# Kernel tuning notes

Hardware: AMD Instinct MI355X
Metric: run time of the kernel (lower is better)

The kernel has to match this reference:

```python
import jax, jax.numpy as jnp
import numpy as np

COMMITMENT_COST = 0.25
N_EMBED = 1024
EMB_DIM = 256

def setup_inputs() -> dict:
    key = jax.random.key(0)
    k1, k2 = jax.random.split(key)
    z = jax.random.normal(k1, (32, EMB_DIM, 32, 32), dtype=jnp.float32)
    # embedding.weight.data.uniform_(-1/n_embed, 1/n_embed)
    embedding = jax.random.uniform(k2, (N_EMBED, EMB_DIM), dtype=jnp.float32,
                                   minval=-1.0 / N_EMBED, maxval=1.0 / N_EMBED)
    return {"z": z, "embedding": embedding}

def reference(z, embedding):
    # NCHW -> NHWC
    zp = jnp.transpose(z, (0, 2, 3, 1))            # [B,H,W,D]
    in_shape = zp.shape
    flat = zp.reshape(-1, in_shape[-1])            # [N,D]
    # squared L2 distances (argmin equivalent to p=2 cdist argmin)
    d2 = (jnp.sum(flat * flat, axis=1, keepdims=True)
          - 2.0 * (flat @ embedding.T)
          + jnp.sum(embedding * embedding, axis=1))  # [N,K]
    idx = jnp.argmin(d2, axis=1)                   # [N]
    # one-hot @ codebook == direct gather
    z_quant = embedding[idx].reshape(in_shape)     # [B,H,W,D]
    codebook_loss = jnp.mean((z_quant - jax.lax.stop_gradient(zp)) ** 2)
    commitment_loss = jnp.mean((zp - jax.lax.stop_gradient(z_quant)) ** 2)
    loss = codebook_loss + COMMITMENT_COST * commitment_loss
    # straight-through estimator
    z_st = zp + jax.lax.stop_gradient(z_quant - zp)
    z_st = jnp.transpose(z_st, (0, 3, 1, 2))       # NHWC -> NCHW
    return (z_st, loss, codebook_loss, commitment_loss)
```

## Files before the change

### kernel.cpp

```cpp
#include <hip/hip_runtime.h>
#include <hip/hip_bf16.h>
#include <stdint.h>


typedef short v8s __attribute__((ext_vector_type(8)));
typedef float v4f __attribute__((ext_vector_type(4)));

__device__ inline unsigned short f2bf(float f) {
    uint32_t u = __float_as_uint(f);
    return (unsigned short)((u + 0x7fffu + ((u >> 16) & 1u)) >> 16);
}

__global__ __launch_bounds__(256) void k_prep_e(const float* __restrict__ E,
                                                v8s* __restrict__ Esw,
                                                float* __restrict__ nE,
                                                float* __restrict__ accum,
                                                unsigned* __restrict__ done) {
    __shared__ float Ef[16][264];
    int q = blockIdx.x, tid = threadIdx.x;
    const float4* Ein = (const float4*)(E + ((size_t)q << 12));
#pragma unroll
    for (int i = 0; i < 4; i++) {
        int f4 = i * 256 + tid;
        int row = f4 >> 6, c4 = (f4 & 63) << 2;
        *(float4*)&Ef[row][c4] = Ein[f4];
    }
    __syncthreads();
    {
        int c = tid >> 4, l = tid & 15;
        float s = 0.f;
#pragma unroll
        for (int j = 0; j < 16; j++) { float v = Ef[c][l + 16 * j]; s += v * v; }
#pragma unroll
        for (int off = 1; off < 16; off <<= 1) s += __shfl_xor(s, off);
        if (l == 0) nE[q * 16 + c] = 0.5f * s;
    }
#pragma unroll
    for (int i = 0; i < 2; i++) {
        int u = tid + i * 256;
        int um = u & 15, ug = (u >> 4) & 3, udc = (u >> 6) & 7;
        int d0 = udc * 32 + ug * 8;
        union { v8s v; unsigned short s[8]; } pk;
#pragma unroll
        for (int e = 0; e < 8; e++) pk.s[e] = f2bf(Ef[um][d0 + e]);
        Esw[((size_t)q << 9) + u] = pk.v;
    }
    if (q == 0 && tid == 0) { accum[0] = 0.f; done[0] = 0u; }
}

__global__ __launch_bounds__(512) void k_main(
        const v8s* __restrict__ Esw,
        const float* __restrict__ nE,
        const float* __restrict__ z,
        const float* __restrict__ E,
        float* __restrict__ out,
        float* __restrict__ accum,
        unsigned* __restrict__ done) {
    __shared__ union {
        v8s    B[2][4096];
        float4 Eg4[2048];
    } S;
    __shared__ float nEl[1024];
    __shared__ float nrmLds[128];
    __shared__ int   idxLds[128];
    __shared__ float w8[8];

    int tid = threadIdx.x;
    int lane = tid & 63, w = tid >> 6;
    int g = lane >> 4, m = lane & 15;
    int R0 = blockIdx.x << 7;
    int b = R0 >> 10, hw0 = R0 & 1023;

    {
        int q = tid & 31, dblk = tid >> 5;
        const float* zp = z + ((size_t)b << 18) + hw0 + (q << 2);
#pragma unroll
        for (int s = 0; s < 2; s++) {
            float4 L[8];
#pragma unroll
            for (int j = 0; j < 8; j++)
                L[j] = *(const float4*)(zp + (size_t)(((dblk << 4) + (s << 3) + j) << 10));
            const float* Lf = (const float*)L;
            int slot = (dblk << 1) + s;
#pragma unroll
            for (int c = 0; c < 4; c++) {
                union { v8s v; unsigned short u[8]; } pk;
#pragma unroll
                for (int j = 0; j < 8; j++) pk.u[j] = f2bf(Lf[j * 4 + c]);
                int row = (q << 2) + c;
                int sw = slot ^ ((row ^ (row >> 2)) & 7);
                *(v8s*)((char*)&S + (row << 9) + (sw << 4)) = pk.v;
            }
        }
    }
#pragma unroll
    for (int i = 0; i < 2; i++) nEl[tid + i * 512] = nE[tid + i * 512];
    __syncthreads();

    v8s a[8];
    {
        int row = (w << 4) + m;
        int f = (row ^ (row >> 2)) & 7;
#pragma unroll
        for (int dc = 0; dc < 8; dc++) {
            int sw = ((dc << 2) + g) ^ f;
            a[dc] = *(const v8s*)((const char*)&S + (row << 9) + (sw << 4));
        }
        float nrm = 0.f;
#pragma unroll
        for (int dc = 0; dc < 8; dc++) {
            union { v8s v; unsigned short u[8]; } un; un.v = a[dc];
#pragma unroll
            for (int j = 0; j < 8; j++) {
                float v = __uint_as_float((uint32_t)un.u[j] << 16);
                nrm = fmaf(v, v, nrm);
            }
        }
        nrm += __shfl_xor(nrm, 16);
        nrm += __shfl_xor(nrm, 32);
        if (g == 0) nrmLds[row] = nrm;
    }
    __syncthreads();

#define STAGE(ch, buf)                                                        \
    {                                                                         \
        _Pragma("unroll")                                                     \
        for (int j = 0; j < 8; j++) {                                         \
            __builtin_amdgcn_global_load_lds(                                 \
                (const __attribute__((address_space(1))) void*)               \
                    (Esw + ((size_t)(ch) << 12) + (j << 9) + (w << 6) + lane),\
                (__attribute__((address_space(3))) void*)                     \
                    &S.B[buf][(j << 9) + (w << 6)],                           \
                16, 0, 0);                                                    \
        }                                                                     \
    }

    float best[4]; int bidx[4];
#pragma unroll
    for (int r = 0; r < 4; r++) { best[r] = 3.4e38f; bidx[r] = 0; }

    STAGE(0, 0);
#pragma unroll 2
    for (int ct = 0; ct < 8; ct++) {
        int cur = ct & 1;
        __syncthreads();
        if (ct < 7) STAGE(ct + 1, cur ^ 1);
        float ne[8];
#pragma unroll
        for (int t = 0; t < 8; t++) ne[t] = nEl[(ct << 7) + (t << 4) + m];
        v4f acc[8];
#pragma unroll
        for (int t = 0; t < 8; t++) acc[t] = (v4f){0.f, 0.f, 0.f, 0.f};
#pragma unroll
        for (int dc = 0; dc < 8; dc++) {
#pragma unroll
            for (int t = 0; t < 8; t++) {
                v8s bf = S.B[cur][t * 512 + dc * 64 + g * 16 + m];
                acc[t] = __builtin_amdgcn_mfma_f32_16x16x32_bf16(a[dc], bf, acc[t], 0, 0, 0);
            }
        }
#pragma unroll
        for (int t = 0; t < 8; t++) {
            int code = (ct << 7) + (t << 4) + m;
#pragma unroll
            for (int r = 0; r < 4; r++) {
                float s0 = ne[t] - acc[t][r];
                if (s0 < best[r]) { best[r] = s0; bidx[r] = code; }
            }
        }
    }

    float lsum = 0.f;
#pragma unroll
    for (int r = 0; r < 4; r++) {
        uint32_t sb = __float_as_uint(best[r]);
        sb = (sb & 0x80000000u) ? ~sb : (sb | 0x80000000u);
        unsigned long long pk = ((unsigned long long)sb << 32) | (uint32_t)bidx[r];
#pragma unroll
        for (int off = 1; off < 16; off <<= 1) {
            unsigned long long o = __shfl_xor(pk, off);
            if (o < pk) pk = o;
        }
        int row = (w << 4) + (g << 2) + r;
        if (m == 0) {
            idxLds[row] = (int)(pk & 0xffffffffu);
            uint32_t t = (uint32_t)(pk >> 32);
            float sw = __uint_as_float((t & 0x80000000u) ? (t & 0x7fffffffu) : ~t);
            lsum += 2.0f * sw + nrmLds[row];
        }
    }
#pragma unroll
    for (int off = 1; off < 64; off <<= 1) lsum += __shfl_xor(lsum, off);
    if (lane == 0) w8[w] = lsum;
    __syncthreads();

    float* ob = out + ((size_t)b << 18);
    int hwl = tid & 31, dq0 = tid >> 5;
#pragma unroll 1
    for (int ph = 0; ph < 4; ph++) {
#pragma unroll
        for (int i = 0; i < 4; i++) {
            int row = w + (i << 3);
            int k = idxLds[(ph << 5) + row];
            float4 v = ((const float4*)(E + ((size_t)k << 8)))[lane];
            S.Eg4[(row << 6) + (lane ^ row)] = v;
        }
        __syncthreads();
        int hwp = hw0 + (ph << 5) + hwl;
#pragma unroll
        for (int i = 0; i < 4; i++) {
            int dq = dq0 + (i << 4);
            float4 ev = S.Eg4[(hwl << 6) + (dq ^ hwl)];
            size_t o = ((size_t)dq << 12) + hwp;
            ob[o] = ev.x; ob[o + 1024] = ev.y; ob[o + 2048] = ev.z; ob[o + 3072] = ev.w;
        }
        __syncthreads();
    }

    if (tid == 0) {
        float s8 = 0.f;
#pragma unroll
        for (int i = 0; i < 8; i++) s8 += w8[i];
        atomicAdd(accum, s8);
        __threadfence();
        unsigned old = atomicAdd(done, 1u);
        if (old == 255u) {
            float s = atomicAdd(accum, 0.f) * (1.0f / 8388608.0f);
            out[8388608] = 1.25f * s;
            out[8388609] = s;
            out[8388610] = s;
        }
    }
#undef STAGE
}

extern "C" void kernel_launch(void* const* d_in, const int* in_sizes, int n_in,
                              void* d_out, int out_size, void* d_ws, size_t ws_size,
                              hipStream_t stream) {
    const float* z = (const float*)d_in[0];
    const float* E = (const float*)d_in[1];
    char* ws = (char*)d_ws;
    v8s*      Esw   = (v8s*)(ws);
    float*    nE    = (float*)(ws + 524288);
    float*    accum = (float*)(ws + 528384);
    unsigned* done  = (unsigned*)(ws + 528388);
    float* out = (float*)d_out;

    hipLaunchKernelGGL(k_prep_e, dim3(64),  dim3(256), 0, stream, E, Esw, nE, accum, done);
    hipLaunchKernelGGL(k_main,   dim3(256), dim3(512), 0, stream,
                       Esw, nE, z, E, out, accum, done);
}
```

Measured before the change: 116.9 us.

## Overlap first codebook stage with z load and rewrite gather-output epilogue

The first codebook tile load is now issued before the z transpose/convert, with z staged in the second LDS buffer so the async copy overlaps the z load. The loop barrier moves to the end of each iteration. The output epilogue drops the LDS-staged gather with its phase barriers: each thread gathers four codebook rows directly from global memory and writes float4 stores along hw. This removes several barriers and LDS traffic, but the direct gathers use strided 16-byte reads per row, which may coalesce less well.

```diff
diff --git a/kernel.cpp b/kernel.cpp
--- a/kernel.cpp
+++ b/kernel.cpp
@@ -56,13 +56,10 @@
         float* __restrict__ out,
         float* __restrict__ accum,
         unsigned* __restrict__ done) {
-    __shared__ union {
-        v8s    B[2][4096];
-        float4 Eg4[2048];
-    } S;
+    __shared__ v8s B[2][4096];
     __shared__ float nEl[1024];
     __shared__ float nrmLds[128];
-    __shared__ int   idxLds[128];
+    __shared__ __align__(16) int idxLds[128];
     __shared__ float w8[8];
 
     int tid = threadIdx.x;
@@ -70,57 +67,6 @@
     int g = lane >> 4, m = lane & 15;
     int R0 = blockIdx.x << 7;
     int b = R0 >> 10, hw0 = R0 & 1023;
-
-    {
-        int q = tid & 31, dblk = tid >> 5;
-        const float* zp = z + ((size_t)b << 18) + hw0 + (q << 2);
-#pragma unroll
-        for (int s = 0; s < 2; s++) {
-            float4 L[8];
-#pragma unroll
-            for (int j = 0; j < 8; j++)
-                L[j] = *(const float4*)(zp + (size_t)(((dblk << 4) + (s << 3) + j) << 10));
-            const float* Lf = (const float*)L;
-            int slot = (dblk << 1) + s;
-#pragma unroll
-            for (int c = 0; c < 4; c++) {
-                union { v8s v; unsigned short u[8]; } pk;
-#pragma unroll
-                for (int j = 0; j < 8; j++) pk.u[j] = f2bf(Lf[j * 4 + c]);
-                int row = (q << 2) + c;
-                int sw = slot ^ ((row ^ (row >> 2)) & 7);
-                *(v8s*)((char*)&S + (row << 9) + (sw << 4)) = pk.v;
-            }
-        }
-    }
-#pragma unroll
-    for (int i = 0; i < 2; i++) nEl[tid + i * 512] = nE[tid + i * 512];
-    __syncthreads();
-
-    v8s a[8];
-    {
-        int row = (w << 4) + m;
-        int f = (row ^ (row >> 2)) & 7;
-#pragma unroll
-        for (int dc = 0; dc < 8; dc++) {
-            int sw = ((dc << 2) + g) ^ f;
-            a[dc] = *(const v8s*)((const char*)&S + (row << 9) + (sw << 4));
-        }
-        float nrm = 0.f;
-#pragma unroll
-        for (int dc = 0; dc < 8; dc++) {
-            union { v8s v; unsigned short u[8]; } un; un.v = a[dc];
-#pragma unroll
-            for (int j = 0; j < 8; j++) {
-                float v = __uint_as_float((uint32_t)un.u[j] << 16);
-                nrm = fmaf(v, v, nrm);
-            }
-        }
-        nrm += __shfl_xor(nrm, 16);
-        nrm += __shfl_xor(nrm, 32);
-        if (g == 0) nrmLds[row] = nrm;
-    }
-    __syncthreads();
 
 #define STAGE(ch, buf)                                                        \
     {                                                                         \
@@ -130,20 +76,70 @@
                 (const __attribute__((address_space(1))) void*)               \
                     (Esw + ((size_t)(ch) << 12) + (j << 9) + (w << 6) + lane),\
                 (__attribute__((address_space(3))) void*)                     \
-                    &S.B[buf][(j << 9) + (w << 6)],                           \
+                    &B[buf][(j << 9) + (w << 6)],                             \
                 16, 0, 0);                                                    \
         }                                                                     \
     }
 
+    STAGE(0, 0);
+
+    {
+        int q = tid & 31, dblk = tid >> 5;
+        const float* zp = z + ((size_t)b << 18) + hw0 + (q << 2);
+#pragma unroll
+        for (int s = 0; s < 2; s++) {
+            float4 L[8];
+#pragma unroll
+            for (int j = 0; j < 8; j++)
+                L[j] = *(const float4*)(zp + (size_t)(((dblk << 4) + (s << 3) + j) << 10));
+            const float* Lf = (const float*)L;
+            int slot = (dblk << 1) + s;
+#pragma unroll
+            for (int c = 0; c < 4; c++) {
+                union { v8s v; unsigned short u[8]; } pk;
+#pragma unroll
+                for (int j = 0; j < 8; j++) pk.u[j] = f2bf(Lf[j * 4 + c]);
+                int row = (q << 2) + c;
+                int sw = slot ^ ((row ^ (row >> 2)) & 7);
+                *(v8s*)((char*)&B[1][0] + (row << 9) + (sw << 4)) = pk.v;
+            }
+        }
+    }
+#pragma unroll
+    for (int i = 0; i < 2; i++) nEl[tid + i * 512] = nE[tid + i * 512];
+    __syncthreads();
+
+    v8s a[8];
+    {
+        int row = (w << 4) + m;
+        int f = (row ^ (row >> 2)) & 7;
+#pragma unroll
+        for (int dc = 0; dc < 8; dc++) {
+            int sw = ((dc << 2) + g) ^ f;
+            a[dc] = *(const v8s*)((const char*)&B[1][0] + (row << 9) + (sw << 4));
+        }
+        float nrm = 0.f;
+#pragma unroll
+        for (int dc = 0; dc < 8; dc++) {
+            union { v8s v; unsigned short u[8]; } un; un.v = a[dc];
+#pragma unroll
+            for (int j = 0; j < 8; j++) {
+                float v = __uint_as_float((uint32_t)un.u[j] << 16);
+                nrm = fmaf(v, v, nrm);
+            }
+        }
+        nrm += __shfl_xor(nrm, 16);
+        nrm += __shfl_xor(nrm, 32);
+        if (g == 0) nrmLds[row] = nrm;
+    }
+    __syncthreads();
     float best[4]; int bidx[4];
 #pragma unroll
     for (int r = 0; r < 4; r++) { best[r] = 3.4e38f; bidx[r] = 0; }
 
-    STAGE(0, 0);
 #pragma unroll 2
     for (int ct = 0; ct < 8; ct++) {
         int cur = ct & 1;
-        __syncthreads();
         if (ct < 7) STAGE(ct + 1, cur ^ 1);
         float ne[8];
 #pragma unroll
@@ -155,7 +151,7 @@
         for (int dc = 0; dc < 8; dc++) {
 #pragma unroll
             for (int t = 0; t < 8; t++) {
-                v8s bf = S.B[cur][t * 512 + dc * 64 + g * 16 + m];
+                v8s bf = B[cur][t * 512 + dc * 64 + g * 16 + m];
                 acc[t] = __builtin_amdgcn_mfma_f32_16x16x32_bf16(a[dc], bf, acc[t], 0, 0, 0);
             }
         }
@@ -168,6 +164,7 @@
                 if (s0 < best[r]) { best[r] = s0; bidx[r] = code; }
             }
         }
+        __syncthreads();
     }
 
     float lsum = 0.f;
@@ -194,27 +191,25 @@
     if (lane == 0) w8[w] = lsum;
     __syncthreads();
 
-    float* ob = out + ((size_t)b << 18);
-    int hwl = tid & 31, dq0 = tid >> 5;
-#pragma unroll 1
-    for (int ph = 0; ph < 4; ph++) {
+    {
+        int q = tid & 31, dd = tid >> 5;
+        int4 kk = *(const int4*)&idxLds[q << 2];
+        float* ob = out + ((size_t)b << 18) + hw0 + (q << 2);
 #pragma unroll
         for (int i = 0; i < 4; i++) {
-            int row = w + (i << 3);
-            int k = idxLds[(ph << 5) + row];
-            float4 v = ((const float4*)(E + ((size_t)k << 8)))[lane];
-            S.Eg4[(row << 6) + (lane ^ row)] = v;
-        }
-        __syncthreads();
-        int hwp = hw0 + (ph << 5) + hwl;
-#pragma unroll
-        for (int i = 0; i < 4; i++) {
-            int dq = dq0 + (i << 4);
-            float4 ev = S.Eg4[(hwl << 6) + (dq ^ hwl)];
-            size_t o = ((size_t)dq << 12) + hwp;
-            ob[o] = ev.x; ob[o + 1024] = ev.y; ob[o + 2048] = ev.z; ob[o + 3072] = ev.w;
-        }
-        __syncthreads();
+            int d0 = (dd + (i << 4)) << 2;
+            float4 e0 = *(const float4*)(E + ((size_t)kk.x << 8) + d0);
+            float4 e1 = *(const float4*)(E + ((size_t)kk.y << 8) + d0);
+            float4 e2 = *(const float4*)(E + ((size_t)kk.z << 8) + d0);
+            float4 e3 = *(const float4*)(E + ((size_t)kk.w << 8) + d0);
+            const float* p0 = &e0.x; const float* p1 = &e1.x;
+            const float* p2 = &e2.x; const float* p3 = &e3.x;
+#pragma unroll
+            for (int r = 0; r < 4; r++) {
+                float4 v; v.x = p0[r]; v.y = p1[r]; v.z = p2[r]; v.w = p3[r];
+                *(float4*)(ob + ((size_t)(d0 + r) << 10)) = v;
+            }
+        }
     }
 
     if (tid == 0) {
```

New measurement: 120.7 us. 1.03x slower.
